# Kernel optimization log

Measured on AMD Instinct MI355X. Metric: run time of the kernel, lower is better.

Reference implementation:

```python
import jax, jax.numpy as jnp
import numpy as np

N_NODES = 100000
N_EDGES = 1600000
HIDDEN = 64
EPS = 1e-5


def setup_inputs() -> dict:
    key = jax.random.key(0)
    ks = jax.random.split(key, 12)
    h = HIDDEN
    inp = {
        'x': jax.random.normal(ks[0], (N_NODES, h), dtype=jnp.float32),
        'edge_index': jax.random.randint(ks[1], (2, N_EDGES), 0, N_NODES, dtype=jnp.int32),
        'message': jax.random.normal(ks[2], (N_EDGES, h), dtype=jnp.float32),
        # node_mlp: Linear(2h->h), BN(h), ReLU, Dropout(identity), Linear(h->h), BN(h), ReLU
        'W1': jax.random.normal(ks[3], (2 * h, h), dtype=jnp.float32) / np.sqrt(2.0 * h),
        'b1': jnp.zeros((h,), jnp.float32),
        'g1': jnp.ones((h,), jnp.float32),
        'be1': jnp.zeros((h,), jnp.float32),
        'W2': jax.random.normal(ks[4], (h, h), dtype=jnp.float32) / np.sqrt(h),
        'b2': jnp.zeros((h,), jnp.float32),
        'g2': jnp.ones((h,), jnp.float32),
        'be2': jnp.zeros((h,), jnp.float32),
        # attention_mlp: Linear(h->1), Sigmoid
        'Wa': jax.random.normal(ks[5], (h, 1), dtype=jnp.float32) / np.sqrt(h),
        'ba': jnp.zeros((1,), jnp.float32),
    }
    return inp


def _scatter_max(msg, idx, n):
    # torch_scatter scatter(..., reduce='max') fills segments with no edges with 0
    agg = jax.ops.segment_max(msg, idx, num_segments=n)  # [N, H], -inf where empty
    cnt = jax.ops.segment_sum(jnp.ones((idx.shape[0],), msg.dtype), idx, num_segments=n)
    return jnp.where(cnt[:, None] > 0, agg, jnp.zeros((), msg.dtype))


def _batchnorm(x, gamma, beta):
    # training-mode BatchNorm1d: batch mean / biased variance
    mu = jnp.mean(x, axis=0)
    var = jnp.mean((x - mu) ** 2, axis=0)
    return (x - mu) * jax.lax.rsqrt(var + EPS) * gamma + beta


def reference(x, edge_index, message, W1, b1, g1, be1, W2, b2, g2, be2, Wa, ba):
    n = x.shape[0]
    row, col = edge_index[0], edge_index[1]
    fwd = _scatter_max(message, col, n)   # [N, H]
    bwd = _scatter_max(message, row, n)   # [N, H]
    out = jnp.concatenate([fwd, bwd], axis=1)          # [N, 2H]
    h1 = jax.nn.relu(_batchnorm(out @ W1 + b1, g1, be1))  # dropout = identity (eval)
    h2 = jax.nn.relu(_batchnorm(h1 @ W2 + b2, g2, be2))   # [N, H]
    att = jax.nn.sigmoid(h2 @ Wa + ba).reshape(-1)          # [N]
    return (h2, att)
```

## Files before the change

kernel.cpp:

```cpp
#include <hip/hip_runtime.h>
#include <hip/hip_bf16.h>
#include <cstdint>
#include <cstddef>

#define HDIM 64
#define EPS 1e-5f
#define BN 128
#define BSH 7
#define NXCD 8
#define BCAPX 2560
#define CURPAD 16
#define SENTE 128u

typedef short bf16x8 __attribute__((ext_vector_type(8)));
typedef float f32x4  __attribute__((ext_vector_type(4)));
typedef float f4v    __attribute__((ext_vector_type(4)));
typedef unsigned u2v __attribute__((ext_vector_type(2)));
typedef unsigned u4v __attribute__((ext_vector_type(4)));

__device__ __forceinline__ unsigned bf16rn(float f) {
    unsigned u = __float_as_uint(f);
    return (u + 0x7FFFu + ((u >> 16) & 1u)) >> 16;
}

__device__ __forceinline__ unsigned flipbf(float f) {
    unsigned h = bf16rn(f);
    return (h & 0x8000u) ? (~h & 0xFFFFu) : (h | 0x8000u);
}

__device__ __forceinline__ unsigned unflipkey(unsigned key) {
    if (key == 0u) return 0u;
    unsigned k = key >> 16;
    return (k & 0x8000u) ? (k & 0x7FFFu) : (~k & 0xFFFFu);
}

__global__ __launch_bounds__(256) void prep_kernel(
    const float* __restrict__ msg, unsigned short* __restrict__ msgB,
    const int* __restrict__ ei, unsigned* __restrict__ bcur,
    unsigned* __restrict__ entries,
    const float* __restrict__ W1, const float* __restrict__ W2,
    unsigned short* __restrict__ W1T, unsigned short* __restrict__ W2T,
    int E, int nblk, int cblocks, int eblocks) {
    int blk = blockIdx.x;
    if (blk < cblocks) {
        size_t i = ((size_t)blk * 256 + threadIdx.x) * 8;
        size_t total = (size_t)E * HDIM;
        if (i < total) {
            f4v a = __builtin_nontemporal_load((const f4v*)&msg[i]);
            f4v b = __builtin_nontemporal_load((const f4v*)&msg[i + 4]);
            u4v o;
            o.x = flipbf(a.x) | (flipbf(a.y) << 16);
            o.y = flipbf(a.z) | (flipbf(a.w) << 16);
            o.z = flipbf(b.x) | (flipbf(b.y) << 16);
            o.w = flipbf(b.z) | (flipbf(b.w) << 16);
            __builtin_nontemporal_store(o, (u4v*)&msgB[i]);
        }
    } else if (blk < cblocks + eblocks) {
        int e = (blk - cblocks) * 256 + threadIdx.x;
        if (e >= E) return;
        unsigned xcd;
        asm volatile("s_getreg_b32 %0, hwreg(HW_REG_XCC_ID)" : "=s"(xcd));
        xcd &= (NXCD - 1);
        int row = ei[e];
        int col = ei[(size_t)E + e];
        unsigned cell1 = (unsigned)(col >> BSH) * NXCD + xcd;
        unsigned cell2 = (unsigned)(nblk + (row >> BSH)) * NXCD + xcd;
        unsigned p1 = atomicAdd(&bcur[(size_t)cell1 * CURPAD], 1u);
        unsigned p2 = atomicAdd(&bcur[(size_t)cell2 * CURPAD], 1u);
        if (p1 < BCAPX)
            entries[(size_t)cell1 * BCAPX + p1] = ((unsigned)e << 8) | (unsigned)(col & (BN - 1));
        if (p2 < BCAPX)
            entries[(size_t)cell2 * BCAPX + p2] = ((unsigned)e << 8) | (unsigned)(row & (BN - 1));
    } else {
        int t = (blk - cblocks - eblocks) * 256 + threadIdx.x;
        if (t < 128 * 64) {
            int k = t >> 6, o = t & 63;
            W1T[o * 128 + k] = (unsigned short)bf16rn(W1[t]);
        } else {
            int t2 = t - 128 * 64;
            if (t2 < 64 * 64) {
                int k = t2 >> 6, o = t2 & 63;
                W2T[o * 64 + k] = (unsigned short)bf16rn(W2[t2]);
            }
        }
    }
}

__global__ __launch_bounds__(256) void binned_max_kernel(
    const unsigned short* __restrict__ msgB, const unsigned* __restrict__ bcur,
    const unsigned* __restrict__ entries,
    unsigned short* __restrict__ fwdB, unsigned short* __restrict__ bwdB,
    int N, int nblk) {
    __shared__ __align__(16) unsigned acc[(BN + 1) * HDIM];
    int tid = threadIdx.x;
    int wave = tid >> 6, lane = tid & 63;
    int b = blockIdx.x;

    {
        u4v z = {};
        u4v* p = (u4v*)acc;
        for (int i = tid; i < (BN + 1) * HDIM / 4; i += 256) p[i] = z;
    }
    __syncthreads();

    unsigned accBase = (unsigned)(size_t)&acc[0];
    unsigned laneOff = accBase + ((unsigned)lane << 2);

    for (int rr = 0; rr < 2; ++rr) {
        int r = wave + rr * 4;
        unsigned cnt = bcur[((size_t)b * NXCD + r) * CURPAD];
        if (cnt > BCAPX) cnt = BCAPX;
        const unsigned* rb = entries + ((size_t)b * NXCD + r) * BCAPX;
        for (unsigned c0 = 0; c0 < cnt; c0 += 64) {
            unsigned myent = (c0 + (unsigned)lane < cnt) ? rb[c0 + lane] : SENTE;
            unsigned rem = cnt - c0;
#pragma unroll
            for (int b16 = 0; b16 < 4; ++b16) {
                if ((unsigned)(b16 * 16) >= rem) break;
                unsigned short v[16];
#pragma unroll
                for (int k = 0; k < 16; ++k) {
                    unsigned ent = __shfl(myent, b16 * 16 + k);
                    v[k] = __builtin_nontemporal_load(&msgB[(size_t)(ent >> 8) * HDIM + lane]);
                }
#pragma unroll
                for (int k = 0; k < 16; ++k) {
                    unsigned ent = __shfl(myent, b16 * 16 + k);
                    unsigned addr = laneOff + ((ent & 255u) << 8);
                    unsigned key = ((unsigned)v[k]) << 16;
                    asm volatile("ds_max_u32 %0, %1" :: "v"(addr), "v"(key));
                }
            }
        }
    }
    asm volatile("" ::: "memory");
    __syncthreads();

    bool fwd = (b < nblk);
    int node0 = (fwd ? b : b - nblk) * BN;
    unsigned short* dst = fwd ? fwdB : bwdB;
    for (int i = tid; i < BN * (HDIM / 4); i += 256) {
        int rrow = i >> 4, c4 = (i & 15) * 4;
        int node = node0 + rrow;
        if (node >= N) continue;
        uint4 a = *(const uint4*)&acc[rrow * HDIM + c4];
        u2v o;
        o.x = unflipkey(a.x) | (unflipkey(a.y) << 16);
        o.y = unflipkey(a.z) | (unflipkey(a.w) << 16);
        *(u2v*)(dst + (size_t)node * HDIM + c4) = o;
    }
}


__global__ __launch_bounds__(256) void gemm1_mfma_kernel(
    const unsigned short* __restrict__ fwdB, const unsigned short* __restrict__ bwdB,
    const unsigned short* __restrict__ W1T, const float* __restrict__ b1,
    float* __restrict__ y1, float* __restrict__ sum1, float* __restrict__ sq1, int N) {
    __shared__ float wsum[4][64], wsq[4][64];
    int tid = threadIdx.x;
    int wave = tid >> 6, lane = tid & 63;
    int lrow = lane & 15, kseg = lane >> 4;
    int rbase = blockIdx.x * 64 + wave * 16;

    bf16x8 bfr[4][4];
#pragma unroll
    for (int nt = 0; nt < 4; ++nt)
#pragma unroll
        for (int kb = 0; kb < 4; ++kb)
            bfr[nt][kb] = *(const bf16x8*)(W1T + (size_t)(nt * 16 + lrow) * 128 + kb * 32 + kseg * 8);

    int r = rbase + lrow;
    bool ok = (r < N);
    size_t ro = (size_t)(ok ? r : 0) * HDIM;
    bf16x8 z = {};
    bf16x8 afr[4];
    afr[0] = *(const bf16x8*)(fwdB + ro + kseg * 8);
    afr[1] = *(const bf16x8*)(fwdB + ro + 32 + kseg * 8);
    afr[2] = *(const bf16x8*)(bwdB + ro + kseg * 8);
    afr[3] = *(const bf16x8*)(bwdB + ro + 32 + kseg * 8);
    if (!ok) { afr[0] = z; afr[1] = z; afr[2] = z; afr[3] = z; }

    f32x4 acc[4] = {};
#pragma unroll
    for (int kb = 0; kb < 4; ++kb)
#pragma unroll
        for (int nt = 0; nt < 4; ++nt)
            acc[nt] = __builtin_amdgcn_mfma_f32_16x16x32_bf16(afr[kb], bfr[nt][kb], acc[nt], 0, 0, 0);

#pragma unroll
    for (int nt = 0; nt < 4; ++nt) {
        int col = nt * 16 + lrow;
        float bias = b1[col];
        float s = 0.f, q = 0.f;
#pragma unroll
        for (int rr = 0; rr < 4; ++rr) {
            int rowi = rbase + kseg * 4 + rr;
            if (rowi < N) {
                float v = acc[nt][rr] + bias;
                y1[(size_t)rowi * HDIM + col] = v;
                s += v; q += v * v;
            }
        }
        s += __shfl_xor(s, 16); s += __shfl_xor(s, 32);
        q += __shfl_xor(q, 16); q += __shfl_xor(q, 32);
        if (kseg == 0) { wsum[wave][col] = s; wsq[wave][col] = q; }
    }
    __syncthreads();
    if (tid < 64) {
        float S = wsum[0][tid] + wsum[1][tid] + wsum[2][tid] + wsum[3][tid];
        float Q = wsq[0][tid] + wsq[1][tid] + wsq[2][tid] + wsq[3][tid];
        atomicAdd(&sum1[tid], S);
        atomicAdd(&sq1[tid], Q);
    }
}

__global__ __launch_bounds__(256) void gemm2_mfma_kernel(
    const float* __restrict__ y1, const float* __restrict__ sum1, const float* __restrict__ sq1,
    const float* __restrict__ g1, const float* __restrict__ be1,
    const unsigned short* __restrict__ W2T, const float* __restrict__ b2,
    float* __restrict__ y2, float* __restrict__ sum2, float* __restrict__ sq2, int N) {
    __shared__ float sc[64], sh[64];
    __shared__ float wsum[4][64], wsq[4][64];
    int tid = threadIdx.x;
    if (tid < 64) {
        float invN = 1.0f / (float)N;
        float mu = sum1[tid] * invN;
        float var = sq1[tid] * invN - mu * mu;
        float rs = rsqrtf(var + EPS);
        float s = rs * g1[tid];
        sc[tid] = s;
        sh[tid] = be1[tid] - mu * s;
    }
    __syncthreads();
    int wave = tid >> 6, lane = tid & 63;
    int lrow = lane & 15, kseg = lane >> 4;
    int rbase = blockIdx.x * 64 + wave * 16;

    bf16x8 bfr[4][2];
#pragma unroll
    for (int nt = 0; nt < 4; ++nt)
#pragma unroll
        for (int kb = 0; kb < 2; ++kb)
            bfr[nt][kb] = *(const bf16x8*)(W2T + (size_t)(nt * 16 + lrow) * 64 + kb * 32 + kseg * 8);

    int r = rbase + lrow;
    size_t ro = (size_t)((r < N) ? r : 0) * HDIM;
    bf16x8 afr[2];
#pragma unroll
    for (int kb = 0; kb < 2; ++kb) {
        const f4v* yp = (const f4v*)(y1 + ro + kb * 32 + kseg * 8);
        f4v u0 = yp[0], u1 = yp[1];
        int k0 = kb * 32 + kseg * 8;
        bf16x8 a;
#pragma unroll
        for (int j = 0; j < 4; ++j) {
            float h0 = fmaxf(fmaf(u0[j], sc[k0 + j], sh[k0 + j]), 0.f);
            float h1 = fmaxf(fmaf(u1[j], sc[k0 + 4 + j], sh[k0 + 4 + j]), 0.f);
            a[j] = (short)bf16rn(h0);
            a[4 + j] = (short)bf16rn(h1);
        }
        afr[kb] = a;
    }

    f32x4 acc[4] = {};
#pragma unroll
    for (int kb = 0; kb < 2; ++kb)
#pragma unroll
        for (int nt = 0; nt < 4; ++nt)
            acc[nt] = __builtin_amdgcn_mfma_f32_16x16x32_bf16(afr[kb], bfr[nt][kb], acc[nt], 0, 0, 0);

#pragma unroll
    for (int nt = 0; nt < 4; ++nt) {
        int col = nt * 16 + lrow;
        float bias = b2[col];
        float s = 0.f, q = 0.f;
#pragma unroll
        for (int rr = 0; rr < 4; ++rr) {
            int rowi = rbase + kseg * 4 + rr;
            if (rowi < N) {
                float v = acc[nt][rr] + bias;
                y2[(size_t)rowi * HDIM + col] = v;
                s += v; q += v * v;
            }
        }
        s += __shfl_xor(s, 16); s += __shfl_xor(s, 32);
        q += __shfl_xor(q, 16); q += __shfl_xor(q, 32);
        if (kseg == 0) { wsum[wave][col] = s; wsq[wave][col] = q; }
    }
    __syncthreads();
    if (tid < 64) {
        float S = wsum[0][tid] + wsum[1][tid] + wsum[2][tid] + wsum[3][tid];
        float Q = wsq[0][tid] + wsq[1][tid] + wsq[2][tid] + wsq[3][tid];
        atomicAdd(&sum2[tid], S);
        atomicAdd(&sq2[tid], Q);
    }
}

__global__ __launch_bounds__(256) void final_kernel(
    const float* __restrict__ y2, const float* __restrict__ sum2, const float* __restrict__ sq2,
    const float* __restrict__ g2, const float* __restrict__ be2,
    const float* __restrict__ Wa, const float* __restrict__ ba,
    float* __restrict__ out_h2, float* __restrict__ out_att, int N) {
    __shared__ float sc[HDIM], sh[HDIM], wa[HDIM];
    __shared__ float bav;
    if (threadIdx.x < HDIM) {
        int c = threadIdx.x;
        float invN = 1.0f / (float)N;
        float mu = sum2[c] * invN;
        float var = sq2[c] * invN - mu * mu;
        float rstd = rsqrtf(var + EPS);
        float s = rstd * g2[c];
        sc[c] = s;
        sh[c] = be2[c] - mu * s;
        wa[c] = Wa[c];
    }
    if (threadIdx.x == 0) bav = ba[0];
    __syncthreads();
    int n = blockIdx.x * 256 + threadIdx.x;
    if (n >= N) return;

    const f4v* p = (const f4v*)&y2[(size_t)n * HDIM];
    f4v* dst = (f4v*)&out_h2[(size_t)n * HDIM];
    float att = bav;
#pragma unroll 1
    for (int kk = 0; kk < 16; ++kk) {
        f4v u = p[kk];
        f4v hv;
#pragma unroll
        for (int j = 0; j < 4; ++j) {
            int k = kk * 4 + j;
            float h = fmaxf(fmaf(u[j], sc[k], sh[k]), 0.0f);
            hv[j] = h;
            att = fmaf(h, wa[k], att);
        }
        dst[kk] = hv;
    }
    out_att[n] = 1.0f / (1.0f + expf(-att));
}

extern "C" void kernel_launch(void* const* d_in, const int* in_sizes, int n_in,
                              void* d_out, int out_size, void* d_ws, size_t ws_size,
                              hipStream_t stream) {
    const int*   ei   = (const int*)d_in[1];
    const float* msg  = (const float*)d_in[2];
    const float* W1   = (const float*)d_in[3];
    const float* b1   = (const float*)d_in[4];
    const float* g1   = (const float*)d_in[5];
    const float* be1  = (const float*)d_in[6];
    const float* W2   = (const float*)d_in[7];
    const float* b2   = (const float*)d_in[8];
    const float* g2   = (const float*)d_in[9];
    const float* be2  = (const float*)d_in[10];
    const float* Wa   = (const float*)d_in[11];
    const float* ba   = (const float*)d_in[12];

    const int N = in_sizes[0] / HDIM;
    const int E = in_sizes[1] / 2;
    const int nblk = (N + BN - 1) / BN;

    unsigned short* fwdB = (unsigned short*)d_ws;
    unsigned short* bwdB = fwdB + (size_t)N * HDIM;
    unsigned short* W1T  = bwdB + (size_t)N * HDIM;
    unsigned short* W2T  = W1T + 8192;
    float*    stats      = (float*)(W2T + 4096);
    unsigned* bcur       = (unsigned*)(stats + 256);
    unsigned* entries    = bcur + (size_t)2 * nblk * NXCD * CURPAD;
    unsigned short* msgB = (unsigned short*)(entries + (size_t)2 * nblk * NXCD * BCAPX);
    float*    y1         = (float*)d_out;
    float*    y2         = (float*)d_ws;
    float*    out_att    = (float*)d_out + (size_t)N * HDIM;

    hipMemsetAsync(stats, 0, 256 * sizeof(float)
                             + (size_t)2 * nblk * NXCD * CURPAD * sizeof(unsigned), stream);

    int cblocks = (int)(((size_t)E * HDIM / 8 + 255) / 256);
    int eblocks = (E + 255) / 256;
    int wblocks = 48;
    prep_kernel<<<cblocks + eblocks + wblocks, 256, 0, stream>>>(
        msg, msgB, ei, bcur, entries, W1, W2, W1T, W2T, E, nblk, cblocks, eblocks);

    binned_max_kernel<<<2 * nblk, 256, 0, stream>>>(msgB, bcur, entries, fwdB, bwdB, N, nblk);

    int G = (N + 63) / 64;
    gemm1_mfma_kernel<<<G, 256, 0, stream>>>(fwdB, bwdB, W1T, b1, y1,
                                             stats, stats + 64, N);
    gemm2_mfma_kernel<<<G, 256, 0, stream>>>(y1, stats, stats + 64, g1, be1,
                                             W2T, b2, y2, stats + 128, stats + 192, N);
    final_kernel<<<(N + 255) / 256, 256, 0, stream>>>(y2, stats + 128, stats + 192,
                                                      g2, be2, Wa, ba,
                                                      (float*)d_out, out_att, N);
}
```

Baseline: 468.7 us.

## Scatter bf16 message rows directly into bin-ordered buffers for contiguous max reads

The compact bf16 message array and the separate edge-entry list are removed. The placement kernel now uses 16 threads per edge: it converts each message row to order-preserving bf16 once and writes it straight into both the forward and the backward bin slots, alongside a 16-bit local node index. The max-reduce kernel then streams rows contiguously instead of gathering them by edge id, so random reads become sequential. In exchange, writes roughly double and become scattered. Bin capacity now comes from workspace size, capped at 1024 per cell; if it comes out too small, edges beyond capacity are silently dropped.

```diff
diff --git a/kernel.cpp b/kernel.cpp
--- a/kernel.cpp
+++ b/kernel.cpp
@@ -8,9 +8,7 @@
 #define BN 128
 #define BSH 7
 #define NXCD 8
-#define BCAPX 2560
 #define CURPAD 16
-#define SENTE 128u
 
 typedef short bf16x8 __attribute__((ext_vector_type(8)));
 typedef float f32x4  __attribute__((ext_vector_type(4)));
@@ -34,30 +32,35 @@
     return (k & 0x8000u) ? (k & 0x7FFFu) : (~k & 0xFFFFu);
 }
 
-__global__ __launch_bounds__(256) void prep_kernel(
-    const float* __restrict__ msg, unsigned short* __restrict__ msgB,
-    const int* __restrict__ ei, unsigned* __restrict__ bcur,
-    unsigned* __restrict__ entries,
+__global__ __launch_bounds__(256) void place_kernel(
+    const float* __restrict__ msg, const int* __restrict__ ei,
+    unsigned* __restrict__ bcur, unsigned short* __restrict__ locs,
+    unsigned short* __restrict__ rows,
     const float* __restrict__ W1, const float* __restrict__ W2,
     unsigned short* __restrict__ W1T, unsigned short* __restrict__ W2T,
-    int E, int nblk, int cblocks, int eblocks) {
+    int E, int nblk, int bcap, int eblocks16) {
     int blk = blockIdx.x;
-    if (blk < cblocks) {
-        size_t i = ((size_t)blk * 256 + threadIdx.x) * 8;
-        size_t total = (size_t)E * HDIM;
-        if (i < total) {
-            f4v a = __builtin_nontemporal_load((const f4v*)&msg[i]);
-            f4v b = __builtin_nontemporal_load((const f4v*)&msg[i + 4]);
-            u4v o;
-            o.x = flipbf(a.x) | (flipbf(a.y) << 16);
-            o.y = flipbf(a.z) | (flipbf(a.w) << 16);
-            o.z = flipbf(b.x) | (flipbf(b.y) << 16);
-            o.w = flipbf(b.z) | (flipbf(b.w) << 16);
-            __builtin_nontemporal_store(o, (u4v*)&msgB[i]);
-        }
-    } else if (blk < cblocks + eblocks) {
-        int e = (blk - cblocks) * 256 + threadIdx.x;
-        if (e >= E) return;
+    if (blk >= eblocks16) {
+        int t = (blk - eblocks16) * 256 + threadIdx.x;
+        if (t < 128 * 64) {
+            int k = t >> 6, o = t & 63;
+            W1T[o * 128 + k] = (unsigned short)bf16rn(W1[t]);
+        } else {
+            int t2 = t - 128 * 64;
+            if (t2 < 64 * 64) {
+                int k = t2 >> 6, o = t2 & 63;
+                W2T[o * 64 + k] = (unsigned short)bf16rn(W2[t2]);
+            }
+        }
+        return;
+    }
+    long long gid = (long long)blk * 256 + threadIdx.x;
+    int e = (int)(gid >> 4);
+    if (e >= E) return;
+    int lane = threadIdx.x & 63;
+    int part = lane & 15;
+    unsigned posF = 0xFFFFFFFFu, posB = 0xFFFFFFFFu;
+    if (part == 0) {
         unsigned xcd;
         asm volatile("s_getreg_b32 %0, hwreg(HW_REG_XCC_ID)" : "=s"(xcd));
         xcd &= (NXCD - 1);
@@ -67,30 +70,28 @@
         unsigned cell2 = (unsigned)(nblk + (row >> BSH)) * NXCD + xcd;
         unsigned p1 = atomicAdd(&bcur[(size_t)cell1 * CURPAD], 1u);
         unsigned p2 = atomicAdd(&bcur[(size_t)cell2 * CURPAD], 1u);
-        if (p1 < BCAPX)
-            entries[(size_t)cell1 * BCAPX + p1] = ((unsigned)e << 8) | (unsigned)(col & (BN - 1));
-        if (p2 < BCAPX)
-            entries[(size_t)cell2 * BCAPX + p2] = ((unsigned)e << 8) | (unsigned)(row & (BN - 1));
-    } else {
-        int t = (blk - cblocks - eblocks) * 256 + threadIdx.x;
-        if (t < 128 * 64) {
-            int k = t >> 6, o = t & 63;
-            W1T[o * 128 + k] = (unsigned short)bf16rn(W1[t]);
-        } else {
-            int t2 = t - 128 * 64;
-            if (t2 < 64 * 64) {
-                int k = t2 >> 6, o = t2 & 63;
-                W2T[o * 64 + k] = (unsigned short)bf16rn(W2[t2]);
-            }
-        }
-    }
+        posF = (p1 < (unsigned)bcap) ? cell1 * (unsigned)bcap + p1 : 0xFFFFFFFFu;
+        posB = (p2 < (unsigned)bcap) ? cell2 * (unsigned)bcap + p2 : 0xFFFFFFFFu;
+        if (posF != 0xFFFFFFFFu) locs[posF] = (unsigned short)(col & (BN - 1));
+        if (posB != 0xFFFFFFFFu) locs[posB] = (unsigned short)(row & (BN - 1));
+    }
+    posF = __shfl(posF, lane & ~15);
+    posB = __shfl(posB, lane & ~15);
+    f4v m = __builtin_nontemporal_load((const f4v*)&msg[(size_t)e * HDIM + part * 4]);
+    u2v b;
+    b.x = flipbf(m.x) | (flipbf(m.y) << 16);
+    b.y = flipbf(m.z) | (flipbf(m.w) << 16);
+    if (posF != 0xFFFFFFFFu)
+        __builtin_nontemporal_store(b, (u2v*)&rows[(size_t)posF * HDIM + part * 4]);
+    if (posB != 0xFFFFFFFFu)
+        __builtin_nontemporal_store(b, (u2v*)&rows[(size_t)posB * HDIM + part * 4]);
 }
 
 __global__ __launch_bounds__(256) void binned_max_kernel(
-    const unsigned short* __restrict__ msgB, const unsigned* __restrict__ bcur,
-    const unsigned* __restrict__ entries,
+    const unsigned short* __restrict__ rows, const unsigned short* __restrict__ locs,
+    const unsigned* __restrict__ bcur,
     unsigned short* __restrict__ fwdB, unsigned short* __restrict__ bwdB,
-    int N, int nblk) {
+    int N, int nblk, int bcap) {
     __shared__ __align__(16) unsigned acc[(BN + 1) * HDIM];
     int tid = threadIdx.x;
     int wave = tid >> 6, lane = tid & 63;
@@ -108,11 +109,14 @@
 
     for (int rr = 0; rr < 2; ++rr) {
         int r = wave + rr * 4;
-        unsigned cnt = bcur[((size_t)b * NXCD + r) * CURPAD];
-        if (cnt > BCAPX) cnt = BCAPX;
-        const unsigned* rb = entries + ((size_t)b * NXCD + r) * BCAPX;
+        size_t cell = (size_t)b * NXCD + r;
+        unsigned cnt = bcur[cell * CURPAD];
+        if (cnt > (unsigned)bcap) cnt = (unsigned)bcap;
+        if (cnt == 0) continue;
+        const unsigned short* lp = locs + cell * (unsigned)bcap;
+        const unsigned short* rp = rows + cell * (unsigned)bcap * HDIM;
         for (unsigned c0 = 0; c0 < cnt; c0 += 64) {
-            unsigned myent = (c0 + (unsigned)lane < cnt) ? rb[c0 + lane] : SENTE;
+            unsigned myloc = (c0 + (unsigned)lane < cnt) ? (unsigned)lp[c0 + lane] : 128u;
             unsigned rem = cnt - c0;
 #pragma unroll
             for (int b16 = 0; b16 < 4; ++b16) {
@@ -120,13 +124,14 @@
                 unsigned short v[16];
 #pragma unroll
                 for (int k = 0; k < 16; ++k) {
-                    unsigned ent = __shfl(myent, b16 * 16 + k);
-                    v[k] = __builtin_nontemporal_load(&msgB[(size_t)(ent >> 8) * HDIM + lane]);
+                    unsigned j = c0 + b16 * 16 + k;
+                    unsigned jc = (j < cnt) ? j : (cnt - 1);
+                    v[k] = __builtin_nontemporal_load(&rp[(size_t)jc * HDIM + lane]);
                 }
 #pragma unroll
                 for (int k = 0; k < 16; ++k) {
-                    unsigned ent = __shfl(myent, b16 * 16 + k);
-                    unsigned addr = laneOff + ((ent & 255u) << 8);
+                    unsigned loc = __shfl(myloc, b16 * 16 + k);
+                    unsigned addr = laneOff + (loc << 8);
                     unsigned key = ((unsigned)v[k]) << 16;
                     asm volatile("ds_max_u32 %0, %1" :: "v"(addr), "v"(key));
                 }
@@ -357,6 +362,7 @@
     const int N = in_sizes[0] / HDIM;
     const int E = in_sizes[1] / 2;
     const int nblk = (N + BN - 1) / BN;
+    const size_t cells = (size_t)2 * nblk * NXCD;
 
     unsigned short* fwdB = (unsigned short*)d_ws;
     unsigned short* bwdB = fwdB + (size_t)N * HDIM;
@@ -364,22 +370,29 @@
     unsigned short* W2T  = W1T + 8192;
     float*    stats      = (float*)(W2T + 4096);
     unsigned* bcur       = (unsigned*)(stats + 256);
-    unsigned* entries    = bcur + (size_t)2 * nblk * NXCD * CURPAD;
-    unsigned short* msgB = (unsigned short*)(entries + (size_t)2 * nblk * NXCD * BCAPX);
+    unsigned short* locs = (unsigned short*)(bcur + cells * CURPAD);
+    size_t locs_off      = (size_t)((char*)locs - (char*)d_ws);
     float*    y1         = (float*)d_out;
     float*    y2         = (float*)d_ws;
     float*    out_att    = (float*)d_out + (size_t)N * HDIM;
 
+    size_t avail = (ws_size > locs_off + 4096) ? ws_size - locs_off - 4096 : 0;
+    int bcap = (int)(avail / (cells * (2 + 128)));
+    bcap &= ~31;
+    if (bcap > 1024) bcap = 1024;
+    if (bcap < 64)   bcap = 64;
+    unsigned short* rowsA = (unsigned short*)
+        ((((size_t)(locs + cells * (size_t)bcap)) + 15) & ~(size_t)15);
+
     hipMemsetAsync(stats, 0, 256 * sizeof(float)
-                             + (size_t)2 * nblk * NXCD * CURPAD * sizeof(unsigned), stream);
-
-    int cblocks = (int)(((size_t)E * HDIM / 8 + 255) / 256);
-    int eblocks = (E + 255) / 256;
-    int wblocks = 48;
-    prep_kernel<<<cblocks + eblocks + wblocks, 256, 0, stream>>>(
-        msg, msgB, ei, bcur, entries, W1, W2, W1T, W2T, E, nblk, cblocks, eblocks);
-
-    binned_max_kernel<<<2 * nblk, 256, 0, stream>>>(msgB, bcur, entries, fwdB, bwdB, N, nblk);
+                             + cells * CURPAD * sizeof(unsigned), stream);
+
+    int eblocks16 = (int)(((long long)E * 16 + 255) / 256);
+    place_kernel<<<eblocks16 + 48, 256, 0, stream>>>(
+        msg, ei, bcur, locs, rowsA, W1, W2, W1T, W2T, E, nblk, bcap, eblocks16);
+
+    binned_max_kernel<<<2 * nblk, 256, 0, stream>>>(rowsA, locs, bcur,
+                                                    fwdB, bwdB, N, nblk, bcap);
 
     int G = (N + 63) / 64;
     gemm1_mfma_kernel<<<G, 256, 0, stream>>>(fwdB, bwdB, W1T, b1, y1,
```

New measurement: 472.5 us. Within noise of the previous version (+0.8%).
